# Kernel tuning notes

Measured on AMD Instinct MI355X. Metric: run time of the kernel, lower is better.

The kernel has to match this reference:

```python
import jax, jax.numpy as jnp
import numpy as np

B, T, D, H = 4, 2048, 1024, 16
HD = D // H  # head_size = 64
EPS = 1e-5


def layernorm(x, g, b):
    mu = jnp.mean(x, axis=-1, keepdims=True)
    var = jnp.var(x, axis=-1, keepdims=True)
    return (x - mu) * jax.lax.rsqrt(var + EPS) * g + b


def setup_inputs() -> dict:
    key = jax.random.key(0)
    ks = jax.random.split(key, 8)
    s = 0.02
    return {
        "x": jax.random.normal(ks[0], (B, T, D), jnp.float32),
        "Wq": jax.random.normal(ks[1], (D, D), jnp.float32) * s,
        "Wk": jax.random.normal(ks[2], (D, D), jnp.float32) * s,
        "Wv": jax.random.normal(ks[3], (D, D), jnp.float32) * s,
        "Wo": jax.random.normal(ks[4], (D, D), jnp.float32) * s,
        "bo": jnp.zeros((D,), jnp.float32),
        "W1": jax.random.normal(ks[5], (D, 4 * D), jnp.float32) * s,
        "b1": jnp.zeros((4 * D,), jnp.float32),
        "W2": jax.random.normal(ks[6], (4 * D, D), jnp.float32) * s,
        "b2": jnp.zeros((D,), jnp.float32),
        "ln1_g": jnp.ones((D,), jnp.float32),
        "ln1_b": jnp.zeros((D,), jnp.float32),
        "ln2_g": jnp.ones((D,), jnp.float32),
        "ln2_b": jnp.zeros((D,), jnp.float32),
    }


def reference(x, Wq, Wk, Wv, Wo, bo, W1, b1, W2, b2, ln1_g, ln1_b, ln2_g, ln2_b):
    # --- multi-head causal self-attention (pre-LN), dropout off (eval) ---
    h = layernorm(x, ln1_g, ln1_b)
    q = jnp.einsum('btd,de->bte', h, Wq).reshape(B, T, H, HD)
    k = jnp.einsum('btd,de->bte', h, Wk).reshape(B, T, H, HD)
    v = jnp.einsum('btd,de->bte', h, Wv).reshape(B, T, H, HD)
    scores = jnp.einsum('bqhd,bkhd->bhqk', q, k) * (HD ** -0.5)
    causal = jnp.tril(jnp.ones((T, T), bool))
    scores = jnp.where(causal, scores, -jnp.inf)
    attn = jax.nn.softmax(scores, axis=-1)
    out = jnp.einsum('bhqk,bkhd->bqhd', attn, v).reshape(B, T, D)
    out = jnp.einsum('btd,de->bte', out, Wo) + bo
    x = x + out
    # --- feed-forward: Linear -> ReLU -> Linear -> ReLU (as in source) ---
    h2 = layernorm(x, ln2_g, ln2_b)
    ff = jax.nn.relu(jnp.einsum('btd,df->btf', h2, W1) + b1)
    ff = jax.nn.relu(jnp.einsum('btf,fd->btd', ff, W2) + b2)
    return x + ff
```

## Files before the change

kernel.cpp:

```cpp
#include <hip/hip_runtime.h>
#include <cstdint>
#include <cstddef>

typedef unsigned short u16;
typedef __attribute__((ext_vector_type(8))) short bf16x8;
typedef __attribute__((ext_vector_type(4))) float f32x4;
typedef __attribute__((address_space(1))) const unsigned int gu32;
typedef __attribute__((address_space(3))) unsigned int lu32;

#define QSCALE 0.1803368801111204f

__device__ __forceinline__ u16 f2bf(float f) {
  uint32_t u = __float_as_uint(f);
  u += 0x7fffu + ((u >> 16) & 1u);
  return (u16)(u >> 16);
}

__global__ __launch_bounds__(256) void transpose_w(const float* __restrict__ W,
                                                   u16* __restrict__ WT,
                                                   int K, int N) {
  __shared__ float t[32][33];
  int n0 = blockIdx.x * 32, k0 = blockIdx.y * 32;
  for (int i = threadIdx.y; i < 32; i += 8)
    t[i][threadIdx.x] = W[(size_t)(k0 + i) * N + n0 + threadIdx.x];
  __syncthreads();
  for (int i = threadIdx.y; i < 32; i += 8)
    WT[(size_t)(n0 + i) * K + k0 + threadIdx.x] = f2bf(t[threadIdx.x][i]);
}

__global__ __launch_bounds__(256) void ln_kernel(const float* __restrict__ x,
                                                 const float* __restrict__ g,
                                                 const float* __restrict__ b,
                                                 u16* __restrict__ out) {
  int row = blockIdx.x;
  const float4 v = *(const float4*)(x + (size_t)row * 1024 + threadIdx.x * 4);
  float s = v.x + v.y + v.z + v.w;
  float ss = v.x * v.x + v.y * v.y + v.z * v.z + v.w * v.w;
#pragma unroll
  for (int d = 1; d < 64; d <<= 1) { s += __shfl_xor(s, d); ss += __shfl_xor(ss, d); }
  __shared__ float rs_[4], rss_[4];
  int wv = threadIdx.x >> 6;
  if ((threadIdx.x & 63) == 0) { rs_[wv] = s; rss_[wv] = ss; }
  __syncthreads();
  s = rs_[0] + rs_[1] + rs_[2] + rs_[3];
  ss = rss_[0] + rss_[1] + rss_[2] + rss_[3];
  float mu = s * (1.f / 1024.f);
  float var = ss * (1.f / 1024.f) - mu * mu;
  float rstd = rsqrtf(var + 1e-5f);
  float4 gv = *(const float4*)(g + threadIdx.x * 4);
  float4 bv = *(const float4*)(b + threadIdx.x * 4);
  uint32_t lo = (uint32_t)f2bf((v.x - mu) * rstd * gv.x + bv.x) |
                ((uint32_t)f2bf((v.y - mu) * rstd * gv.y + bv.y) << 16);
  uint32_t hi = (uint32_t)f2bf((v.z - mu) * rstd * gv.z + bv.z) |
                ((uint32_t)f2bf((v.w - mu) * rstd * gv.w + bv.w) << 16);
  uint2 o; o.x = lo; o.y = hi;
  *(uint2*)(out + (size_t)row * 1024 + threadIdx.x * 4) = o;
}

#define STAGEA(slot, tnext, is)                                               \
  __builtin_amdgcn_global_load_lds(                                           \
      (gu32*)((const char*)(A + (size_t)(bm * 256 + (is) * 64 + srow) * K +   \
                            (size_t)(tnext) * 64) + ssw),                     \
      (lu32*)&lds[(slot) * 24576 + (is) * 4096 + wid * 512], 16, 0, 0)
#define STAGEB(slot, tnext, is)                                               \
  __builtin_amdgcn_global_load_lds(                                           \
      (gu32*)((const char*)(BT + (size_t)(bn * 128 + (is) * 64 + srow) * K +  \
                            (size_t)(tnext) * 64) + ssw),                     \
      (lu32*)&lds[(slot) * 24576 + 16384 + (is) * 4096 + wid * 512], 16, 0, 0)

template <int MODE>
__global__ __launch_bounds__(512, 2) void gemm8p(
    const u16* __restrict__ A, const u16* __restrict__ BT,
    int M, int N, int K,
    const float* __restrict__ bias, const float* __restrict__ resid,
    float* __restrict__ outf,
    u16* __restrict__ ob0, u16* __restrict__ ob1, u16* __restrict__ ob2) {
  __shared__ __align__(16) u16 lds[73728];
  const int tid = threadIdx.x, lane = tid & 63, wid = tid >> 6;
  const int wr = wid >> 1, wc = wid & 1;
  const int bm = blockIdx.y, bn = blockIdx.x;
  const int l15 = lane & 15, lhi = lane >> 4;
  const int srow = tid >> 3;
  const int ssw = ((tid & 7) * 16) ^ ((srow & 7) << 4);
  const int cs0 = (lhi * 8) ^ ((l15 & 7) << 3);
  const int cs1 = (32 + lhi * 8) ^ ((l15 & 7) << 3);
  const int arow = (wr * 64 + l15) * 64;
  const int brow = (wc * 64 + l15) * 64;

  f32x4 acc[4][4];
#pragma unroll
  for (int i = 0; i < 4; ++i)
#pragma unroll
    for (int j = 0; j < 4; ++j) acc[i][j] = (f32x4){0.f, 0.f, 0.f, 0.f};

  const int NT = K >> 6;

#pragma unroll
  for (int t0 = 0; t0 < 2; ++t0) {
    STAGEA(t0, t0, 0); STAGEA(t0, t0, 1); STAGEA(t0, t0, 2); STAGEA(t0, t0, 3);
    STAGEB(t0, t0, 0); STAGEB(t0, t0, 1);
  }
  asm volatile("s_waitcnt vmcnt(6)" ::: "memory");
  __builtin_amdgcn_s_barrier();

  int s = 0, sn = 2;
  for (int t = 0; t < NT; ++t) {
    const bool hasPre = (t + 2) < NT;
    const int aoff = s * 24576, boff = s * 24576 + 16384;

    bf16x8 bfr[4][2], afr[2][2];
#pragma unroll
    for (int ni = 0; ni < 4; ++ni) {
      bfr[ni][0] = *(const bf16x8*)&lds[boff + brow + ni * 1024 + cs0];
      bfr[ni][1] = *(const bf16x8*)&lds[boff + brow + ni * 1024 + cs1];
    }
    afr[0][0] = *(const bf16x8*)&lds[aoff + arow + cs0];
    afr[0][1] = *(const bf16x8*)&lds[aoff + arow + cs1];
    afr[1][0] = *(const bf16x8*)&lds[aoff + arow + 1024 + cs0];
    afr[1][1] = *(const bf16x8*)&lds[aoff + arow + 1024 + cs1];
    if (hasPre) { STAGEA(sn, t + 2, 0); STAGEA(sn, t + 2, 1); STAGEB(sn, t + 2, 0); }
    __builtin_amdgcn_s_barrier();
    __builtin_amdgcn_s_setprio(1);
#pragma unroll
    for (int ks = 0; ks < 2; ++ks)
#pragma unroll
      for (int ml = 0; ml < 2; ++ml)
#pragma unroll
        for (int ni = 0; ni < 4; ++ni)
          acc[ml][ni] = __builtin_amdgcn_mfma_f32_16x16x32_bf16(afr[ml][ks], bfr[ni][ks], acc[ml][ni], 0, 0, 0);
    __builtin_amdgcn_s_setprio(0);
    __builtin_amdgcn_s_barrier();

    afr[0][0] = *(const bf16x8*)&lds[aoff + arow + 2048 + cs0];
    afr[0][1] = *(const bf16x8*)&lds[aoff + arow + 2048 + cs1];
    afr[1][0] = *(const bf16x8*)&lds[aoff + arow + 3072 + cs0];
    afr[1][1] = *(const bf16x8*)&lds[aoff + arow + 3072 + cs1];
    if (hasPre) { STAGEA(sn, t + 2, 2); STAGEA(sn, t + 2, 3); STAGEB(sn, t + 2, 1); }
    __builtin_amdgcn_s_barrier();
    __builtin_amdgcn_s_setprio(1);
#pragma unroll
    for (int ks = 0; ks < 2; ++ks)
#pragma unroll
      for (int ml = 0; ml < 2; ++ml)
#pragma unroll
        for (int ni = 0; ni < 4; ++ni)
          acc[2 + ml][ni] = __builtin_amdgcn_mfma_f32_16x16x32_bf16(afr[ml][ks], bfr[ni][ks], acc[2 + ml][ni], 0, 0, 0);
    __builtin_amdgcn_s_setprio(0);
    if (hasPre) {
      asm volatile("s_waitcnt vmcnt(6)" ::: "memory");
    } else if (t + 1 < NT) {
      asm volatile("s_waitcnt vmcnt(0)" ::: "memory");
    }
    __builtin_amdgcn_s_barrier();

    s = (s == 2) ? 0 : s + 1;
    sn = (sn == 2) ? 0 : sn + 1;
  }

  if (MODE == 0 || MODE == 2) {
    char* ep = (char*)lds;
    const bool vmode = (MODE == 0) && (bn >= 16);
    if (vmode) {
#pragma unroll
      for (int mi = 0; mi < 4; ++mi)
#pragma unroll
        for (int ni = 0; ni < 4; ++ni) {
          uint32_t lo, hi;
          asm("v_cvt_pk_bf16_f32 %0, %1, %2"
              : "=v"(lo) : "v"(acc[mi][ni][0]), "v"(acc[mi][ni][1]));
          asm("v_cvt_pk_bf16_f32 %0, %1, %2"
              : "=v"(hi) : "v"(acc[mi][ni][2]), "v"(acc[mi][ni][3]));
          uint2 pk; pk.x = lo; pk.y = hi;
          int c_local = wc * 64 + ni * 16 + l15;
          int rb = wr * 64 + mi * 16 + lhi * 4;
          *(uint2*)(ep + c_local * 528 + rb * 2) = pk;
        }
    } else {
      const float sc = (MODE == 0 && bn < 8) ? QSCALE : 1.f;
#pragma unroll
      for (int mi = 0; mi < 4; ++mi)
#pragma unroll
        for (int ni = 0; ni < 4; ++ni) {
          int c_local = wc * 64 + ni * 16 + l15;
          int rb = wr * 64 + mi * 16 + lhi * 4;
          float bv = (MODE == 2) ? bias[bn * 128 + c_local] : 0.f;
#pragma unroll
          for (int r = 0; r < 4; ++r) {
            float v = acc[mi][ni][r];
            if (MODE == 2) v = fmaxf(v + bv, 0.f);
            else v *= sc;
            *(u16*)(ep + (rb + r) * 272 + c_local * 2) = f2bf(v);
          }
        }
    }
    __syncthreads();
    if (vmode) {
#pragma unroll
      for (int i = 0; i < 8; ++i) {
        int idx = i * 512 + tid;
        int c = idx >> 5, tc = idx & 31;
        uint4 d4 = *(const uint4*)(ep + c * 528 + tc * 16);
        int cm = bn * 128 + c - 2048, hh = cm >> 6, dd = cm & 63;
        size_t bh = (size_t)((bm >> 3) * 16 + hh);
        int t0 = (bm & 7) * 256;
        *(uint4*)&ob2[(bh * 64 + dd) * 2048 + t0 + tc * 8] = d4;
      }
    } else {
#pragma unroll
      for (int i = 0; i < 8; ++i) {
        int idx = i * 512 + tid;
        int row = idx >> 4, cc = idx & 15;
        uint4 d4 = *(const uint4*)(ep + row * 272 + cc * 16);
        size_t rg = (size_t)(bm * 256 + row);
        if (MODE == 2) {
          *(uint4*)&ob0[rg * N + bn * 128 + cc * 8] = d4;
        } else {
          int colg = bn * 128 + cc * 8;
          if (colg < 1024)
            *(uint4*)&ob0[rg * 1024 + colg] = d4;
          else
            *(uint4*)&ob1[rg * 1024 + colg - 1024] = d4;
        }
      }
    }
  } else {
#pragma unroll
    for (int mi = 0; mi < 4; ++mi) {
#pragma unroll
      for (int ni = 0; ni < 4; ++ni) {
        int col = bn * 128 + wc * 64 + ni * 16 + l15;
        int rbase = bm * 256 + wr * 64 + mi * 16 + lhi * 4;
#pragma unroll
        for (int r = 0; r < 4; ++r) {
          float v = acc[mi][ni][r];
          int rg = rbase + r;
          if (MODE == 1) {
            outf[(size_t)rg * N + col] = v + bias[col] + resid[(size_t)rg * N + col];
          } else {
            outf[(size_t)rg * N + col] = fmaxf(v + bias[col], 0.f) + resid[(size_t)rg * N + col];
          }
        }
      }
    }
  }
}

__global__ __launch_bounds__(512) void attn_kernel(
    const u16* __restrict__ Qb, const u16* __restrict__ Kb,
    const u16* __restrict__ VTb, u16* __restrict__ O) {
  const int p = blockIdx.x;
  const int bh = blockIdx.y;
  const int b = bh >> 4, h = bh & 15;
  const u16* Q = Qb + (size_t)b * 2048 * 1024 + h * 64;
  const u16* Kn = Kb + (size_t)b * 2048 * 1024 + h * 64;
  const u16* VT = VTb + (size_t)bh * 64 * 2048;
  const int tid = threadIdx.x, lane = tid & 63, wv = tid >> 6;
  const int l15 = lane & 15, lhi = lane >> 4;
  const int srow = tid >> 3;
  const int scol16 = (tid & 7) * 16;
  const int sw = scol16 ^ ((srow & 7) << 4);
  const int rswz = (l15 & 7) << 4;
  const int cb0 = (lhi * 16) ^ rswz;
  const int cb1 = (64 + lhi * 16) ^ rswz;

  __shared__ __align__(16) u16 KV[2][2][4096];
  __shared__ u16 Ps[8][16 * 72];

#define STAGEKV(slot, kt)                                                     \
  do {                                                                        \
    __builtin_amdgcn_global_load_lds(                                         \
        (gu32*)((const char*)(Kn + (size_t)((kt)*64 + srow) * 1024) + sw),    \
        (lu32*)&KV[slot][0][wv * 512], 16, 0, 0);                             \
    __builtin_amdgcn_global_load_lds(                                         \
        (gu32*)((const char*)(VT + (size_t)srow * 2048 + (kt)*64) + sw),      \
        (lu32*)&KV[slot][1][wv * 512], 16, 0, 0);                             \
  } while (0)

#pragma unroll
  for (int pass = 0; pass < 2; ++pass) {
    const int chunk = pass ? p : (15 - p);
    const int qbase = chunk * 128 + wv * 16;
    const int nkt = 2 * chunk + 2;

    bf16x8 qf[2];
#pragma unroll
    for (int ks = 0; ks < 2; ++ks)
      qf[ks] = *(const bf16x8*)&Q[(size_t)(qbase + l15) * 1024 + ks * 32 + lhi * 8];

    f32x4 o[4];
#pragma unroll
    for (int f = 0; f < 4; ++f) o[f] = (f32x4){0.f, 0.f, 0.f, 0.f};
    float m = -1e30f;
    float l = 0.f;

    __syncthreads();
    STAGEKV(0, 0);

    for (int kt = 0; kt < nkt; ++kt) {
      const int cs = kt & 1;
      asm volatile("s_waitcnt vmcnt(0)" ::: "memory");
      __syncthreads();
      if (kt + 1 < nkt) STAGEKV(cs ^ 1, kt + 1);

      if (kt * 64 <= qbase + 15) {
        const char* Kbase = (const char*)&KV[cs][0][0];
        const char* Vbase = (const char*)&KV[cs][1][0];

        f32x4 s[4];
#pragma unroll
        for (int jt = 0; jt < 4; ++jt) s[jt] = (f32x4){0.f, 0.f, 0.f, 0.f};
        __builtin_amdgcn_s_setprio(1);
#pragma unroll
        for (int ks = 0; ks < 2; ++ks) {
          const int cbyte = ks ? cb1 : cb0;
#pragma unroll
          for (int jt = 0; jt < 4; ++jt) {
            bf16x8 kf = *(const bf16x8*)(Kbase + (jt * 16 + l15) * 128 + cbyte);
            s[jt] = __builtin_amdgcn_mfma_f32_16x16x32_bf16(kf, qf[ks], s[jt], 0, 0, 0);
          }
        }
        __builtin_amdgcn_s_setprio(0);

        if (kt * 64 + 63 > qbase) {
          int qg = qbase + l15;
#pragma unroll
          for (int jt = 0; jt < 4; ++jt)
#pragma unroll
            for (int r = 0; r < 4; ++r) {
              int kg = kt * 64 + jt * 16 + lhi * 4 + r;
              if (kg > qg) s[jt][r] = -1e30f;
            }
        }

        float mr = fmaxf(fmaxf(s[0][0], s[0][1]), fmaxf(s[0][2], s[0][3]));
#pragma unroll
        for (int jt = 1; jt < 4; ++jt)
          mr = fmaxf(mr, fmaxf(fmaxf(s[jt][0], s[jt][1]), fmaxf(s[jt][2], s[jt][3])));
        mr = fmaxf(mr, __shfl_xor(mr, 16));
        mr = fmaxf(mr, __shfl_xor(mr, 32));
        if (__any(mr > m + 8.f)) {
          float mn = fmaxf(m, mr);
          float sc = exp2f(m - mn);
          l *= sc;
          m = mn;
#pragma unroll
          for (int r = 0; r < 4; ++r) {
            float so = __shfl(sc, lhi * 4 + r);
#pragma unroll
            for (int f = 0; f < 4; ++f) o[f][r] *= so;
          }
        }

        float rs = 0.f;
#pragma unroll
        for (int jt = 0; jt < 4; ++jt)
#pragma unroll
          for (int r = 0; r < 4; ++r) {
            float pv = exp2f(s[jt][r] - m);
            s[jt][r] = pv;
            rs += pv;
          }
        rs += __shfl_xor(rs, 16);
        rs += __shfl_xor(rs, 32);
        l += rs;

#pragma unroll
        for (int jt = 0; jt < 4; ++jt) {
          uint32_t lo, hi;
          asm("v_cvt_pk_bf16_f32 %0, %1, %2"
              : "=v"(lo) : "v"(s[jt][0]), "v"(s[jt][1]));
          asm("v_cvt_pk_bf16_f32 %0, %1, %2"
              : "=v"(hi) : "v"(s[jt][2]), "v"(s[jt][3]));
          uint2 pk; pk.x = lo; pk.y = hi;
          *(uint2*)&Ps[wv][l15 * 72 + jt * 16 + lhi * 4] = pk;
        }
        __builtin_amdgcn_s_setprio(1);
#pragma unroll
        for (int ks = 0; ks < 2; ++ks) {
          const int cbyte = ks ? cb1 : cb0;
          bf16x8 pf = *(const bf16x8*)&Ps[wv][l15 * 72 + ks * 32 + lhi * 8];
#pragma unroll
          for (int f = 0; f < 4; ++f) {
            bf16x8 vfr = *(const bf16x8*)(Vbase + (f * 16 + l15) * 128 + cbyte);
            o[f] = __builtin_amdgcn_mfma_f32_16x16x32_bf16(pf, vfr, o[f], 0, 0, 0);
          }
        }
        __builtin_amdgcn_s_setprio(0);
      }
    }

#pragma unroll
    for (int r = 0; r < 4; ++r) {
      float ld = __shfl(l, lhi * 4 + r);
      float inv = 1.f / ld;
      int t = qbase + lhi * 4 + r;
#pragma unroll
      for (int f = 0; f < 4; ++f)
        O[((size_t)(b * 2048 + t)) * 1024 + h * 64 + f * 16 + l15] = f2bf(o[f][r] * inv);
    }
  }
#undef STAGEKV
}

extern "C" void kernel_launch(void* const* d_in, const int* in_sizes, int n_in,
                              void* d_out, int out_size, void* d_ws, size_t ws_size,
                              hipStream_t stream) {
  const float* x   = (const float*)d_in[0];
  const float* Wq  = (const float*)d_in[1];
  const float* Wk  = (const float*)d_in[2];
  const float* Wv  = (const float*)d_in[3];
  const float* Wo  = (const float*)d_in[4];
  const float* bo  = (const float*)d_in[5];
  const float* W1  = (const float*)d_in[6];
  const float* b1  = (const float*)d_in[7];
  const float* W2  = (const float*)d_in[8];
  const float* b2  = (const float*)d_in[9];
  const float* g1  = (const float*)d_in[10];
  const float* be1 = (const float*)d_in[11];
  const float* g2  = (const float*)d_in[12];
  const float* be2 = (const float*)d_in[13];

  char* p = (char*)d_ws;
  auto alloc = [&](size_t bytes) {
    char* r = p;
    p += (bytes + 255) & ~(size_t)255;
    return r;
  };
  u16* WqkvT = (u16*)alloc(3072ull * 1024 * 2);
  u16* WoT   = (u16*)alloc(1024ull * 1024 * 2);
  u16* W1T   = (u16*)alloc(4096ull * 1024 * 2);
  u16* W2T   = (u16*)alloc(1024ull * 4096 * 2);
  u16* hln   = (u16*)alloc(8192ull * 1024 * 2);
  u16* Qbuf  = (u16*)alloc(8192ull * 1024 * 2);
  u16* Kbuf  = (u16*)alloc(8192ull * 1024 * 2);
  u16* VTbuf = (u16*)alloc(8192ull * 1024 * 2);
  float* x2  = (float*)alloc(8192ull * 1024 * 4);
  u16* ff1   = (u16*)alloc(8192ull * 4096 * 2);
  u16* Oattn = hln;
  u16* h2    = Qbuf;
  if ((size_t)(p - (char*)d_ws) > ws_size) return;

  dim3 tb(32, 8);
  transpose_w<<<dim3(32, 32), tb, 0, stream>>>(Wq, WqkvT, 1024, 1024);
  transpose_w<<<dim3(32, 32), tb, 0, stream>>>(Wk, WqkvT + 1024 * 1024, 1024, 1024);
  transpose_w<<<dim3(32, 32), tb, 0, stream>>>(Wv, WqkvT + 2048 * 1024, 1024, 1024);
  transpose_w<<<dim3(32, 32), tb, 0, stream>>>(Wo, WoT, 1024, 1024);
  transpose_w<<<dim3(128, 32), tb, 0, stream>>>(W1, W1T, 1024, 4096);
  transpose_w<<<dim3(32, 128), tb, 0, stream>>>(W2, W2T, 4096, 1024);

  ln_kernel<<<8192, 256, 0, stream>>>(x, g1, be1, hln);

  gemm8p<0><<<dim3(24, 32), 512, 0, stream>>>(hln, WqkvT, 8192, 3072, 1024,
                                              nullptr, nullptr, nullptr,
                                              Qbuf, Kbuf, VTbuf);

  attn_kernel<<<dim3(8, 64), 512, 0, stream>>>(Qbuf, Kbuf, VTbuf, Oattn);

  gemm8p<1><<<dim3(8, 32), 512, 0, stream>>>(Oattn, WoT, 8192, 1024, 1024,
                                             bo, x, x2, nullptr, nullptr, nullptr);

  ln_kernel<<<8192, 256, 0, stream>>>(x2, g2, be2, h2);

  gemm8p<2><<<dim3(32, 32), 512, 0, stream>>>(h2, W1T, 8192, 4096, 1024,
                                              b1, nullptr, nullptr, ff1, nullptr, nullptr);

  gemm8p<3><<<dim3(8, 32), 512, 0, stream>>>(ff1, W2T, 8192, 1024, 4096,
                                             b2, x2, (float*)d_out, nullptr, nullptr, nullptr);
}
```

Baseline: 403.9 us.

## Add 256x256-tile GEMM kernel for FFN up-projection with fused bias-ReLU epilogue

Replaces the 256x128 gemm8p MODE 2 launch for the W1 projection with a new gemm256 kernel that computes 256x256 output tiles. Each warp owns a 128x64 sub-tile, and operand tiles are double-buffered in LDS through global_load_lds. The larger tile is meant to raise arithmetic intensity and cut global reloads of A and B. In exchange it uses 128KB of LDS and 128 accumulator registers per lane, which limits occupancy. With only 512 blocks the grid fills fewer waves, and the epilogue is split into two halves that share the LDS buffer.

New measurement: 393.0 us. 1.03x faster.

```diff
diff --git a/kernel.cpp b/kernel.cpp
--- a/kernel.cpp
+++ b/kernel.cpp
@@ -157,9 +157,9 @@
     sn = (sn == 2) ? 0 : sn + 1;
   }
 
-  if (MODE == 0 || MODE == 2) {
+  if (MODE == 0) {
     char* ep = (char*)lds;
-    const bool vmode = (MODE == 0) && (bn >= 16);
+    const bool vmode = (bn >= 16);
     if (vmode) {
 #pragma unroll
       for (int mi = 0; mi < 4; ++mi)
@@ -176,20 +176,16 @@
           *(uint2*)(ep + c_local * 528 + rb * 2) = pk;
         }
     } else {
-      const float sc = (MODE == 0 && bn < 8) ? QSCALE : 1.f;
+      const float sc = (bn < 8) ? QSCALE : 1.f;
 #pragma unroll
       for (int mi = 0; mi < 4; ++mi)
 #pragma unroll
         for (int ni = 0; ni < 4; ++ni) {
           int c_local = wc * 64 + ni * 16 + l15;
           int rb = wr * 64 + mi * 16 + lhi * 4;
-          float bv = (MODE == 2) ? bias[bn * 128 + c_local] : 0.f;
 #pragma unroll
           for (int r = 0; r < 4; ++r) {
-            float v = acc[mi][ni][r];
-            if (MODE == 2) v = fmaxf(v + bv, 0.f);
-            else v *= sc;
-            *(u16*)(ep + (rb + r) * 272 + c_local * 2) = f2bf(v);
+            *(u16*)(ep + (rb + r) * 272 + c_local * 2) = f2bf(acc[mi][ni][r] * sc);
           }
         }
     }
@@ -212,15 +208,11 @@
         int row = idx >> 4, cc = idx & 15;
         uint4 d4 = *(const uint4*)(ep + row * 272 + cc * 16);
         size_t rg = (size_t)(bm * 256 + row);
-        if (MODE == 2) {
-          *(uint4*)&ob0[rg * N + bn * 128 + cc * 8] = d4;
-        } else {
-          int colg = bn * 128 + cc * 8;
-          if (colg < 1024)
-            *(uint4*)&ob0[rg * 1024 + colg] = d4;
-          else
-            *(uint4*)&ob1[rg * 1024 + colg - 1024] = d4;
-        }
+        int colg = bn * 128 + cc * 8;
+        if (colg < 1024)
+          *(uint4*)&ob0[rg * 1024 + colg] = d4;
+        else
+          *(uint4*)&ob1[rg * 1024 + colg - 1024] = d4;
       }
     }
   } else {
@@ -241,6 +233,117 @@
           }
         }
       }
+    }
+  }
+}
+
+#define SA256(buf, t, is)                                                     \
+  __builtin_amdgcn_global_load_lds(                                           \
+      (gu32*)((const char*)(A + (size_t)(bm * 256 + (is) * 64 + srow) * K +   \
+                            (size_t)(t) * 64) + ssw),                         \
+      (lu32*)&lds[(buf) * 32768 + (is) * 4096 + wid * 512], 16, 0, 0)
+#define SB256(buf, t, is)                                                     \
+  __builtin_amdgcn_global_load_lds(                                           \
+      (gu32*)((const char*)(BT + (size_t)(bn * 256 + (is) * 64 + srow) * K +  \
+                            (size_t)(t) * 64) + ssw),                         \
+      (lu32*)&lds[(buf) * 32768 + 16384 + (is) * 4096 + wid * 512], 16, 0, 0)
+
+__global__ __launch_bounds__(512, 2) void gemm256(
+    const u16* __restrict__ A, const u16* __restrict__ BT,
+    int M, int N, int K,
+    const float* __restrict__ bias, u16* __restrict__ out) {
+  __shared__ __align__(16) u16 lds[65536];
+  const int tid = threadIdx.x, lane = tid & 63, wid = tid >> 6;
+  const int wr = wid >> 2, wc = wid & 3;
+  const int bm = blockIdx.y, bn = blockIdx.x;
+  const int l15 = lane & 15, lhi = lane >> 4;
+  const int srow = tid >> 3;
+  const int ssw = ((tid & 7) * 16) ^ ((srow & 7) << 4);
+  const int rsw = (l15 & 7) << 4;
+  const int cbyte0 = (lhi * 16) ^ rsw;
+  const int cbyte1 = (64 + lhi * 16) ^ rsw;
+
+  f32x4 acc[8][4];
+#pragma unroll
+  for (int i = 0; i < 8; ++i)
+#pragma unroll
+    for (int j = 0; j < 4; ++j) acc[i][j] = (f32x4){0.f, 0.f, 0.f, 0.f};
+
+  const int NT = K >> 6;
+
+#pragma unroll
+  for (int is = 0; is < 4; ++is) SA256(0, 0, is);
+#pragma unroll
+  for (int is = 0; is < 4; ++is) SB256(0, 0, is);
+  asm volatile("s_waitcnt vmcnt(0)" ::: "memory");
+  __builtin_amdgcn_s_barrier();
+
+  for (int t = 0; t < NT; ++t) {
+    const int buf = t & 1;
+    const char* Ap = (const char*)lds + buf * 65536;
+    const char* Bp = Ap + 32768;
+    const bool hasNext = (t + 1) < NT;
+
+    bf16x8 bfr[4], afr[4];
+#pragma unroll
+    for (int ph = 0; ph < 4; ++ph) {
+      const int ks = ph >> 1, mg = ph & 1;
+      const int cb = ks ? cbyte1 : cbyte0;
+      if (mg == 0) {
+#pragma unroll
+        for (int ni = 0; ni < 4; ++ni)
+          bfr[ni] = *(const bf16x8*)(Bp + (wc * 64 + ni * 16 + l15) * 128 + cb);
+      }
+#pragma unroll
+      for (int i = 0; i < 4; ++i)
+        afr[i] = *(const bf16x8*)(Ap + (wr * 128 + (mg * 4 + i) * 16 + l15) * 128 + cb);
+      if (ph == 0 && hasNext) {
+        SA256(buf ^ 1, t + 1, 0); SA256(buf ^ 1, t + 1, 1);
+        SA256(buf ^ 1, t + 1, 2); SA256(buf ^ 1, t + 1, 3);
+        SB256(buf ^ 1, t + 1, 0); SB256(buf ^ 1, t + 1, 1);
+        SB256(buf ^ 1, t + 1, 2); SB256(buf ^ 1, t + 1, 3);
+      }
+      __builtin_amdgcn_s_barrier();
+      __builtin_amdgcn_s_setprio(1);
+#pragma unroll
+      for (int i = 0; i < 4; ++i)
+#pragma unroll
+        for (int ni = 0; ni < 4; ++ni)
+          acc[mg * 4 + i][ni] = __builtin_amdgcn_mfma_f32_16x16x32_bf16(afr[i], bfr[ni], acc[mg * 4 + i][ni], 0, 0, 0);
+      __builtin_amdgcn_s_setprio(0);
+      if (ph == 3 && hasNext) asm volatile("s_waitcnt vmcnt(0)" ::: "memory");
+      __builtin_amdgcn_s_barrier();
+    }
+  }
+
+  char* ep = (char*)lds;
+#pragma unroll
+  for (int h = 0; h < 2; ++h) {
+    __syncthreads();
+    if (wr == h) {
+#pragma unroll
+      for (int ni = 0; ni < 4; ++ni) {
+        int c_local = wc * 64 + ni * 16 + l15;
+        float bv = bias[bn * 256 + c_local];
+#pragma unroll
+        for (int mi = 0; mi < 8; ++mi) {
+          int rb = mi * 16 + lhi * 4;
+#pragma unroll
+          for (int r = 0; r < 4; ++r) {
+            float v = fmaxf(acc[mi][ni][r] + bv, 0.f);
+            *(u16*)(ep + (rb + r) * 528 + c_local * 2) = f2bf(v);
+          }
+        }
+      }
+    }
+    __syncthreads();
+#pragma unroll
+    for (int i = 0; i < 8; ++i) {
+      int idx = i * 512 + tid;
+      int row = idx >> 5, cc = idx & 31;
+      uint4 d4 = *(const uint4*)(ep + row * 528 + cc * 16);
+      size_t rg = (size_t)(bm * 256 + h * 128 + row);
+      *(uint4*)&out[rg * (size_t)N + bn * 256 + cc * 8] = d4;
     }
   }
 }
@@ -461,8 +564,7 @@
 
   ln_kernel<<<8192, 256, 0, stream>>>(x2, g2, be2, h2);
 
-  gemm8p<2><<<dim3(32, 32), 512, 0, stream>>>(h2, W1T, 8192, 4096, 1024,
-                                              b1, nullptr, nullptr, ff1, nullptr, nullptr);
+  gemm256<<<dim3(16, 32), 512, 0, stream>>>(h2, W1T, 8192, 4096, 1024, b1, ff1);
 
   gemm8p<3><<<dim3(8, 32), 512, 0, stream>>>(ff1, W2T, 8192, 1024, 4096,
                                              b2, x2, (float*)d_out, nullptr, nullptr, nullptr);
```

## Replace 256x128 pipelined GEMM with 128x128 single-buffer GEMM and XCD swizzle

Applied to the files above, without the earlier changes.

Swaps the 512-thread, 256x128-tile, triple-buffered GEMM for a 256-thread 128x128-tile kernel. The new kernel uses a single LDS stage with two barriers per K step, targets four blocks per CU, and remaps block IDs so neighbouring tiles land on the same XCD. The epilogues now stage through the smaller LDS in halves or quarters and use vectorised float4 bias and residual stores. The aim is more occupancy and better L2 locality. In exchange it loses the software prefetch overlap of global loads with MFMA work.

After: 394.0 us. 2.5% less time.

```diff
diff --git a/kernel.cpp b/kernel.cpp
--- a/kernel.cpp
+++ b/kernel.cpp
@@ -14,6 +14,15 @@
   uint32_t u = __float_as_uint(f);
   u += 0x7fffu + ((u >> 16) & 1u);
   return (u16)(u >> 16);
+}
+
+__device__ __forceinline__ void xcd_swz(int& bn, int& bm) {
+  int gx = (int)gridDim.x;
+  int n = gx * (int)gridDim.y;
+  int lid = (int)blockIdx.x + gx * (int)blockIdx.y;
+  int nid = (lid & 7) * (n >> 3) + (lid >> 3);
+  bn = nid % gx;
+  bm = nid / gx;
 }
 
 __global__ __launch_bounds__(256) void transpose_w(const float* __restrict__ W,
@@ -57,35 +66,37 @@
   *(uint2*)(out + (size_t)row * 1024 + threadIdx.x * 4) = o;
 }
 
-#define STAGEA(slot, tnext, is)                                               \
+#define G128A(is)                                                             \
   __builtin_amdgcn_global_load_lds(                                           \
-      (gu32*)((const char*)(A + (size_t)(bm * 256 + (is) * 64 + srow) * K +   \
-                            (size_t)(tnext) * 64) + ssw),                     \
-      (lu32*)&lds[(slot) * 24576 + (is) * 4096 + wid * 512], 16, 0, 0)
-#define STAGEB(slot, tnext, is)                                               \
+      (gu32*)((const char*)(A + (size_t)(bm * 128 + (is) * 32 + srow) * K +   \
+                            (size_t)kt * 64) + ssw),                          \
+      (lu32*)&lds[(is) * 2048 + wid * 512], 16, 0, 0)
+#define G128B(is)                                                             \
   __builtin_amdgcn_global_load_lds(                                           \
-      (gu32*)((const char*)(BT + (size_t)(bn * 128 + (is) * 64 + srow) * K +  \
-                            (size_t)(tnext) * 64) + ssw),                     \
-      (lu32*)&lds[(slot) * 24576 + 16384 + (is) * 4096 + wid * 512], 16, 0, 0)
+      (gu32*)((const char*)(BT + (size_t)(bn * 128 + (is) * 32 + srow) * K +  \
+                            (size_t)kt * 64) + ssw),                          \
+      (lu32*)&lds[8192 + (is) * 2048 + wid * 512], 16, 0, 0)
 
 template <int MODE>
-__global__ __launch_bounds__(512, 2) void gemm8p(
+__global__ __launch_bounds__(256, 4) void g128(
     const u16* __restrict__ A, const u16* __restrict__ BT,
     int M, int N, int K,
     const float* __restrict__ bias, const float* __restrict__ resid,
     float* __restrict__ outf,
     u16* __restrict__ ob0, u16* __restrict__ ob1, u16* __restrict__ ob2) {
-  __shared__ __align__(16) u16 lds[73728];
+  __shared__ __align__(16) u16 lds[16384];
   const int tid = threadIdx.x, lane = tid & 63, wid = tid >> 6;
   const int wr = wid >> 1, wc = wid & 1;
-  const int bm = blockIdx.y, bn = blockIdx.x;
+  int bn, bm;
+  xcd_swz(bn, bm);
   const int l15 = lane & 15, lhi = lane >> 4;
   const int srow = tid >> 3;
   const int ssw = ((tid & 7) * 16) ^ ((srow & 7) << 4);
-  const int cs0 = (lhi * 8) ^ ((l15 & 7) << 3);
-  const int cs1 = (32 + lhi * 8) ^ ((l15 & 7) << 3);
-  const int arow = (wr * 64 + l15) * 64;
-  const int brow = (wc * 64 + l15) * 64;
+  const int swz = (l15 & 7) << 4;
+  const int cb0 = (lhi * 16) ^ swz;
+  const int cb1 = (64 + lhi * 16) ^ swz;
+  const char* Ab = (const char*)lds;
+  const char* Bb = (const char*)lds + 16384;
 
   f32x4 acc[4][4];
 #pragma unroll
@@ -95,151 +106,140 @@
 
   const int NT = K >> 6;
 
-#pragma unroll
-  for (int t0 = 0; t0 < 2; ++t0) {
-    STAGEA(t0, t0, 0); STAGEA(t0, t0, 1); STAGEA(t0, t0, 2); STAGEA(t0, t0, 3);
-    STAGEB(t0, t0, 0); STAGEB(t0, t0, 1);
+  for (int kt = 0; kt < NT; ++kt) {
+    __syncthreads();
+    G128A(0); G128A(1); G128A(2); G128A(3);
+    G128B(0); G128B(1); G128B(2); G128B(3);
+    __syncthreads();
+#pragma unroll
+    for (int ks = 0; ks < 2; ++ks) {
+      const int cb = ks ? cb1 : cb0;
+      bf16x8 af[4], bf[4];
+#pragma unroll
+      for (int mi = 0; mi < 4; ++mi)
+        af[mi] = *(const bf16x8*)(Ab + (wr * 64 + mi * 16 + l15) * 128 + cb);
+#pragma unroll
+      for (int ni = 0; ni < 4; ++ni)
+        bf[ni] = *(const bf16x8*)(Bb + (wc * 64 + ni * 16 + l15) * 128 + cb);
+#pragma unroll
+      for (int mi = 0; mi < 4; ++mi)
+#pragma unroll
+        for (int ni = 0; ni < 4; ++ni)
+          acc[mi][ni] = __builtin_amdgcn_mfma_f32_16x16x32_bf16(af[mi], bf[ni], acc[mi][ni], 0, 0, 0);
+    }
   }
-  asm volatile("s_waitcnt vmcnt(6)" ::: "memory");
-  __builtin_amdgcn_s_barrier();
-
-  int s = 0, sn = 2;
-  for (int t = 0; t < NT; ++t) {
-    const bool hasPre = (t + 2) < NT;
-    const int aoff = s * 24576, boff = s * 24576 + 16384;
-
-    bf16x8 bfr[4][2], afr[2][2];
-#pragma unroll
-    for (int ni = 0; ni < 4; ++ni) {
-      bfr[ni][0] = *(const bf16x8*)&lds[boff + brow + ni * 1024 + cs0];
-      bfr[ni][1] = *(const bf16x8*)&lds[boff + brow + ni * 1024 + cs1];
-    }
-    afr[0][0] = *(const bf16x8*)&lds[aoff + arow + cs0];
-    afr[0][1] = *(const bf16x8*)&lds[aoff + arow + cs1];
-    afr[1][0] = *(const bf16x8*)&lds[aoff + arow + 1024 + cs0];
-    afr[1][1] = *(const bf16x8*)&lds[aoff + arow + 1024 + cs1];
-    if (hasPre) { STAGEA(sn, t + 2, 0); STAGEA(sn, t + 2, 1); STAGEB(sn, t + 2, 0); }
-    __builtin_amdgcn_s_barrier();
-    __builtin_amdgcn_s_setprio(1);
-#pragma unroll
-    for (int ks = 0; ks < 2; ++ks)
-#pragma unroll
-      for (int ml = 0; ml < 2; ++ml)
-#pragma unroll
-        for (int ni = 0; ni < 4; ++ni)
-          acc[ml][ni] = __builtin_amdgcn_mfma_f32_16x16x32_bf16(afr[ml][ks], bfr[ni][ks], acc[ml][ni], 0, 0, 0);
-    __builtin_amdgcn_s_setprio(0);
-    __builtin_amdgcn_s_barrier();
-
-    afr[0][0] = *(const bf16x8*)&lds[aoff + arow + 2048 + cs0];
-    afr[0][1] = *(const bf16x8*)&lds[aoff + arow + 2048 + cs1];
-    afr[1][0] = *(const bf16x8*)&lds[aoff + arow + 3072 + cs0];
-    afr[1][1] = *(const bf16x8*)&lds[aoff + arow + 3072 + cs1];
-    if (hasPre) { STAGEA(sn, t + 2, 2); STAGEA(sn, t + 2, 3); STAGEB(sn, t + 2, 1); }
-    __builtin_amdgcn_s_barrier();
-    __builtin_amdgcn_s_setprio(1);
-#pragma unroll
-    for (int ks = 0; ks < 2; ++ks)
-#pragma unroll
-      for (int ml = 0; ml < 2; ++ml)
-#pragma unroll
-        for (int ni = 0; ni < 4; ++ni)
-          acc[2 + ml][ni] = __builtin_amdgcn_mfma_f32_16x16x32_bf16(afr[ml][ks], bfr[ni][ks], acc[2 + ml][ni], 0, 0, 0);
-    __builtin_amdgcn_s_setprio(0);
-    if (hasPre) {
-      asm volatile("s_waitcnt vmcnt(6)" ::: "memory");
-    } else if (t + 1 < NT) {
-      asm volatile("s_waitcnt vmcnt(0)" ::: "memory");
-    }
-    __builtin_amdgcn_s_barrier();
-
-    s = (s == 2) ? 0 : s + 1;
-    sn = (sn == 2) ? 0 : sn + 1;
-  }
-
-  if (MODE == 0 || MODE == 2) {
-    char* ep = (char*)lds;
-    const bool vmode = (MODE == 0) && (bn >= 16);
-    if (vmode) {
-#pragma unroll
-      for (int mi = 0; mi < 4; ++mi)
-#pragma unroll
-        for (int ni = 0; ni < 4; ++ni) {
-          uint32_t lo, hi;
-          asm("v_cvt_pk_bf16_f32 %0, %1, %2"
-              : "=v"(lo) : "v"(acc[mi][ni][0]), "v"(acc[mi][ni][1]));
-          asm("v_cvt_pk_bf16_f32 %0, %1, %2"
-              : "=v"(hi) : "v"(acc[mi][ni][2]), "v"(acc[mi][ni][3]));
-          uint2 pk; pk.x = lo; pk.y = hi;
-          int c_local = wc * 64 + ni * 16 + l15;
-          int rb = wr * 64 + mi * 16 + lhi * 4;
-          *(uint2*)(ep + c_local * 528 + rb * 2) = pk;
-        }
-    } else {
-      const float sc = (MODE == 0 && bn < 8) ? QSCALE : 1.f;
-#pragma unroll
-      for (int mi = 0; mi < 4; ++mi)
-#pragma unroll
-        for (int ni = 0; ni < 4; ++ni) {
-          int c_local = wc * 64 + ni * 16 + l15;
-          int rb = wr * 64 + mi * 16 + lhi * 4;
-          float bv = (MODE == 2) ? bias[bn * 128 + c_local] : 0.f;
-#pragma unroll
-          for (int r = 0; r < 4; ++r) {
-            float v = acc[mi][ni][r];
-            if (MODE == 2) v = fmaxf(v + bv, 0.f);
-            else v *= sc;
-            *(u16*)(ep + (rb + r) * 272 + c_local * 2) = f2bf(v);
-          }
-        }
-    }
-    __syncthreads();
-    if (vmode) {
-#pragma unroll
-      for (int i = 0; i < 8; ++i) {
-        int idx = i * 512 + tid;
-        int c = idx >> 5, tc = idx & 31;
-        uint4 d4 = *(const uint4*)(ep + c * 528 + tc * 16);
-        int cm = bn * 128 + c - 2048, hh = cm >> 6, dd = cm & 63;
-        size_t bh = (size_t)((bm >> 3) * 16 + hh);
-        int t0 = (bm & 7) * 256;
+
+  char* ep = (char*)lds;
+  if (MODE == 0 && bn >= 16) {
+#pragma unroll
+    for (int h = 0; h < 2; ++h) {
+      __syncthreads();
+      if (wc == h) {
+#pragma unroll
+        for (int mi = 0; mi < 4; ++mi)
+#pragma unroll
+          for (int ni = 0; ni < 4; ++ni) {
+            uint32_t lo, hi;
+            asm("v_cvt_pk_bf16_f32 %0, %1, %2"
+                : "=v"(lo) : "v"(acc[mi][ni][0]), "v"(acc[mi][ni][1]));
+            asm("v_cvt_pk_bf16_f32 %0, %1, %2"
+                : "=v"(hi) : "v"(acc[mi][ni][2]), "v"(acc[mi][ni][3]));
+            uint2 pk; pk.x = lo; pk.y = hi;
+            int c_local = ni * 16 + l15;
+            int rb = wr * 64 + mi * 16 + lhi * 4;
+            *(uint2*)(ep + c_local * 264 + rb * 2) = pk;
+          }
+      }
+      __syncthreads();
+#pragma unroll
+      for (int it = 0; it < 4; ++it) {
+        int idx = it * 256 + tid;
+        int c = idx >> 4, tc = idx & 15;
+        uint4 d4 = *(const uint4*)(ep + c * 264 + tc * 16);
+        int cm = bn * 128 + h * 64 + c - 2048, hh = cm >> 6, dd = cm & 63;
+        size_t bh = (size_t)((bm >> 4) * 16 + hh);
+        int t0 = (bm & 15) * 128;
         *(uint4*)&ob2[(bh * 64 + dd) * 2048 + t0 + tc * 8] = d4;
       }
-    } else {
-#pragma unroll
-      for (int i = 0; i < 8; ++i) {
-        int idx = i * 512 + tid;
+    }
+  } else if (MODE == 0 || MODE == 2) {
+    const float sc = (MODE == 0 && bn < 8) ? QSCALE : 1.f;
+#pragma unroll
+    for (int h = 0; h < 2; ++h) {
+      __syncthreads();
+      if (wr == h) {
+#pragma unroll
+        for (int mi = 0; mi < 4; ++mi)
+#pragma unroll
+          for (int ni = 0; ni < 4; ++ni) {
+            int c_local = wc * 64 + ni * 16 + l15;
+            int rb = mi * 16 + lhi * 4;
+            float bv = (MODE == 2) ? bias[bn * 128 + c_local] : 0.f;
+#pragma unroll
+            for (int r = 0; r < 4; ++r) {
+              float v = acc[mi][ni][r];
+              v = (MODE == 2) ? fmaxf(v + bv, 0.f) : v * sc;
+              *(u16*)(ep + (rb + r) * 272 + c_local * 2) = f2bf(v);
+            }
+          }
+      }
+      __syncthreads();
+#pragma unroll
+      for (int it = 0; it < 4; ++it) {
+        int idx = it * 256 + tid;
         int row = idx >> 4, cc = idx & 15;
         uint4 d4 = *(const uint4*)(ep + row * 272 + cc * 16);
-        size_t rg = (size_t)(bm * 256 + row);
+        size_t rg = (size_t)(bm * 128 + h * 64 + row);
+        int colg = bn * 128 + cc * 8;
         if (MODE == 2) {
-          *(uint4*)&ob0[rg * N + bn * 128 + cc * 8] = d4;
+          *(uint4*)&ob0[rg * (size_t)N + colg] = d4;
+        } else if (colg < 1024) {
+          *(uint4*)&ob0[rg * 1024 + colg] = d4;
         } else {
-          int colg = bn * 128 + cc * 8;
-          if (colg < 1024)
-            *(uint4*)&ob0[rg * 1024 + colg] = d4;
-          else
-            *(uint4*)&ob1[rg * 1024 + colg - 1024] = d4;
+          *(uint4*)&ob1[rg * 1024 + colg - 1024] = d4;
         }
       }
     }
   } else {
-#pragma unroll
-    for (int mi = 0; mi < 4; ++mi) {
-#pragma unroll
-      for (int ni = 0; ni < 4; ++ni) {
-        int col = bn * 128 + wc * 64 + ni * 16 + l15;
-        int rbase = bm * 256 + wr * 64 + mi * 16 + lhi * 4;
-#pragma unroll
-        for (int r = 0; r < 4; ++r) {
-          float v = acc[mi][ni][r];
-          int rg = rbase + r;
-          if (MODE == 1) {
-            outf[(size_t)rg * N + col] = v + bias[col] + resid[(size_t)rg * N + col];
-          } else {
-            outf[(size_t)rg * N + col] = fmaxf(v + bias[col], 0.f) + resid[(size_t)rg * N + col];
-          }
-        }
+    float* epf = (float*)lds;
+#pragma unroll
+    for (int q = 0; q < 4; ++q) {
+      __syncthreads();
+      if (wr == (q >> 1)) {
+#pragma unroll
+        for (int mh = 0; mh < 2; ++mh) {
+          int mi = (q & 1) * 2 + mh;
+#pragma unroll
+          for (int ni = 0; ni < 4; ++ni) {
+            int c_local = wc * 64 + ni * 16 + l15;
+            int rl = mh * 16 + lhi * 4;
+#pragma unroll
+            for (int r = 0; r < 4; ++r)
+              epf[(rl + r) * 132 + c_local] = acc[mi][ni][r];
+          }
+        }
+      }
+      __syncthreads();
+#pragma unroll
+      for (int it = 0; it < 4; ++it) {
+        int idx = it * 256 + tid;
+        int row = idx >> 5, cc = idx & 31;
+        float4 v = *(const float4*)&epf[row * 132 + cc * 4];
+        int colg = bn * 128 + cc * 4;
+        size_t rg = (size_t)(bm * 128 + q * 32 + row);
+        float4 bv = *(const float4*)&bias[colg];
+        float4 rv = *(const float4*)&resid[rg * (size_t)N + colg];
+        float4 o4;
+        if (MODE == 1) {
+          o4.x = v.x + bv.x + rv.x; o4.y = v.y + bv.y + rv.y;
+          o4.z = v.z + bv.z + rv.z; o4.w = v.w + bv.w + rv.w;
+        } else {
+          o4.x = fmaxf(v.x + bv.x, 0.f) + rv.x;
+          o4.y = fmaxf(v.y + bv.y, 0.f) + rv.y;
+          o4.z = fmaxf(v.z + bv.z, 0.f) + rv.z;
+          o4.w = fmaxf(v.w + bv.w, 0.f) + rv.w;
+        }
+        *(float4*)&outf[rg * (size_t)N + colg] = o4;
       }
     }
   }
@@ -450,20 +450,20 @@
 
   ln_kernel<<<8192, 256, 0, stream>>>(x, g1, be1, hln);
 
-  gemm8p<0><<<dim3(24, 32), 512, 0, stream>>>(hln, WqkvT, 8192, 3072, 1024,
-                                              nullptr, nullptr, nullptr,
-                                              Qbuf, Kbuf, VTbuf);
+  g128<0><<<dim3(24, 64), 256, 0, stream>>>(hln, WqkvT, 8192, 3072, 1024,
+                                            nullptr, nullptr, nullptr,
+                                            Qbuf, Kbuf, VTbuf);
 
   attn_kernel<<<dim3(8, 64), 512, 0, stream>>>(Qbuf, Kbuf, VTbuf, Oattn);
 
-  gemm8p<1><<<dim3(8, 32), 512, 0, stream>>>(Oattn, WoT, 8192, 1024, 1024,
-                                             bo, x, x2, nullptr, nullptr, nullptr);
+  g128<1><<<dim3(8, 64), 256, 0, stream>>>(Oattn, WoT, 8192, 1024, 1024,
+                                           bo, x, x2, nullptr, nullptr, nullptr);
 
   ln_kernel<<<8192, 256, 0, stream>>>(x2, g2, be2, h2);
 
-  gemm8p<2><<<dim3(32, 32), 512, 0, stream>>>(h2, W1T, 8192, 4096, 1024,
-                                              b1, nullptr, nullptr, ff1, nullptr, nullptr);
-
-  gemm8p<3><<<dim3(8, 32), 512, 0, stream>>>(ff1, W2T, 8192, 1024, 4096,
-                                             b2, x2, (float*)d_out, nullptr, nullptr, nullptr);
-}
+  g128<2><<<dim3(32, 64), 256, 0, stream>>>(h2, W1T, 8192, 4096, 1024,
+                                            b1, nullptr, nullptr, ff1, nullptr, nullptr);
+
+  g128<3><<<dim3(8, 64), 256, 0, stream>>>(ff1, W2T, 8192, 1024, 4096,
+                                           b2, x2, (float*)d_out, nullptr, nullptr, nullptr);
+}
```
